# Kernel optimization log

Hardware: AMD Instinct MI355X
Metric: run time of the kernel (lower is better)

Reference implementation:

```python
import jax, jax.numpy as jnp
import numpy as np

H, DK, DV = 16, 64, 64

def setup_inputs() -> dict:
    key = jax.random.key(0)
    ks = jax.random.split(key, 5)
    S, E = 2048, 1024
    return {
        "x": jax.random.normal(ks[0], (S, E), jnp.float32),
        "Wq": jax.random.normal(ks[1], (H * DK, E), jnp.float32) * 0.02,
        "Wk": jax.random.normal(ks[2], (H * DK, E), jnp.float32) * 0.02,
        "Wv": jax.random.normal(ks[3], (H * DV, E), jnp.float32) * 0.02,
        "Wo": jax.random.normal(ks[4], (H * DV, H * DV), jnp.float32) * 0.02,
    }

def reference(x, Wq, Wk, Wv, Wo):
    S = x.shape[0]
    # Fused QKV projections (equivalent to per-head Linear with concatenated weights)
    Q = (x @ Wq.T).reshape(S, H, DK).transpose(1, 0, 2)  # [H,S,dk]
    K = (x @ Wk.T).reshape(S, H, DK).transpose(1, 0, 2)  # [H,S,dk]
    V = (x @ Wv.T).reshape(S, H, DV).transpose(1, 0, 2)  # [H,S,dv]
    scale = 1.0 / np.sqrt(DK).astype(np.float32)
    scores = jnp.einsum('hsd,htd->hst', Q, K) * scale    # [H,S,S]
    weights = jax.nn.softmax(scores, axis=-1)
    A = jnp.einsum('hst,htv->hsv', weights, V)           # [H,S,dv]
    A1 = A.transpose(1, 0, 2).reshape(S, H * DV)         # concat heads on last dim
    return A1 @ Wo.T
```

## Files before the change

kernel.cpp:

```cpp
#include <hip/hip_runtime.h>
#include <hip/hip_bf16.h>
#include <stdint.h>

typedef uint16_t u16;
typedef uint32_t u32;
typedef float    f32x4  __attribute__((ext_vector_type(4)));
typedef __bf16   bf16x8 __attribute__((ext_vector_type(8)));
typedef uint16_t u16x8  __attribute__((ext_vector_type(8)));
typedef uint16_t u16x4  __attribute__((ext_vector_type(4)));
typedef uint32_t u32x4  __attribute__((ext_vector_type(4)));

#define HH 16
#define SS 2048
#define EE 1024
#define DD 64

__device__ inline u16 f2bf(float f) {
  uint32_t u = __builtin_bit_cast(uint32_t, f);
  u += 0x7fff + ((u >> 16) & 1);
  return (u16)(u >> 16);
}
__device__ inline float bf2f(u16 b) {
  return __builtin_bit_cast(float, (uint32_t)b << 16);
}

__device__ inline u32 cvtpk(float lo, float hi) {
  u32 r;
  asm("v_cvt_pk_bf16_f32 %0, %1, %2" : "=v"(r) : "v"(lo), "v"(hi));
  return r;
}

__device__ inline void gload_lds16(const void* g, void* l) {
  __builtin_amdgcn_global_load_lds(
      (const __attribute__((address_space(1))) uint32_t*)g,
      (__attribute__((address_space(3))) uint32_t*)l, 16, 0, 0);
}

__global__ __launch_bounds__(256) void convert_kernel(
    const float* __restrict__ x,  const float* __restrict__ wq,
    const float* __restrict__ wk, const float* __restrict__ wv,
    const float* __restrict__ wo,
    u16* __restrict__ xb, u16* __restrict__ wqkvb, u16* __restrict__ wob) {
  const int64_t M1 = 1024 * 1024;
  int64_t e = ((int64_t)blockIdx.x * 256 + threadIdx.x) * 4;
  const float* src; u16* dst; int64_t off;
  if (e < 2 * M1)      { src = x;  dst = xb;           off = e; }
  else if (e < 3 * M1) { src = wq; dst = wqkvb;        off = e - 2 * M1; }
  else if (e < 4 * M1) { src = wk; dst = wqkvb + M1;   off = e - 3 * M1; }
  else if (e < 5 * M1) { src = wv; dst = wqkvb + 2*M1; off = e - 4 * M1; }
  else                 { src = wo; dst = wob;          off = e - 5 * M1; }
  float4 v = *(const float4*)(src + off);
  u16x4 o;
  o[0] = f2bf(v.x); o[1] = f2bf(v.y); o[2] = f2bf(v.z); o[3] = f2bf(v.w);
  *(u16x4*)(dst + off) = o;
}

template <int EPI, int K, int N>
__global__ __launch_bounds__(256, 4) void gemm_kernel(
    const u16* __restrict__ A, const u16* __restrict__ B,
    u16* __restrict__ q_ws, u16* __restrict__ k_ws, u16* __restrict__ vt_ws,
    float* __restrict__ Cout) {
  constexpr int BM = 64, BN = 128, BK = 64;
  __shared__ __align__(16) u16 As[BM * BK];
  __shared__ __align__(16) u16 Bs[BN * BK];
  const int t = threadIdx.x;
  const int lane = t & 63, w = t >> 6;
  const int wr = w >> 1, wc = w & 1;
  const int fr = lane & 15, fg = lane >> 4;

  const int nwg = gridDim.x * gridDim.y;
  const int bid = blockIdx.y * gridDim.x + blockIdx.x;
  const int swz = (bid & 7) * (nwg >> 3) + (bid >> 3);
  const int m0 = (swz / gridDim.x) * BM, n0 = (swz % gridDim.x) * BN;

  f32x4 acc[2][4] = {};

  for (int k0 = 0; k0 < K; k0 += BK) {
#pragma unroll
    for (int it = 0; it < 2; ++it) {
      const int c = t + it * 256, row = c >> 3, sch = (c & 7) ^ (row & 7);
      gload_lds16(A + (int64_t)(m0 + row) * K + k0 + sch * 8,
                  As + (c & ~63) * 8);
    }
#pragma unroll
    for (int it = 0; it < 4; ++it) {
      const int c = t + it * 256, row = c >> 3, sch = (c & 7) ^ (row & 7);
      gload_lds16(B + (int64_t)(n0 + row) * K + k0 + sch * 8,
                  Bs + (c & ~63) * 8);
    }
    __syncthreads();
    bf16x8 af[2][2], bfr[4][2];
#pragma unroll
    for (int mi = 0; mi < 2; ++mi)
#pragma unroll
      for (int kc = 0; kc < 2; ++kc) {
        const int row = wr * 32 + mi * 16 + fr;
        const int cc = (kc * 4 + fg) ^ (row & 7);
        af[mi][kc] = __builtin_bit_cast(bf16x8, *(const u16x8*)&As[row * 64 + cc * 8]);
      }
#pragma unroll
    for (int ni = 0; ni < 4; ++ni)
#pragma unroll
      for (int kc = 0; kc < 2; ++kc) {
        const int row = wc * 64 + ni * 16 + fr;
        const int cc = (kc * 4 + fg) ^ (row & 7);
        bfr[ni][kc] = __builtin_bit_cast(bf16x8, *(const u16x8*)&Bs[row * 64 + cc * 8]);
      }
#pragma unroll
    for (int kc = 0; kc < 2; ++kc)
#pragma unroll
      for (int mi = 0; mi < 2; ++mi)
#pragma unroll
        for (int ni = 0; ni < 4; ++ni)
          acc[mi][ni] = __builtin_amdgcn_mfma_f32_16x16x32_bf16(
              af[mi][kc], bfr[ni][kc], acc[mi][ni], 0, 0, 0);
    __syncthreads();
  }

#pragma unroll
  for (int mi = 0; mi < 2; ++mi)
#pragma unroll
    for (int ni = 0; ni < 4; ++ni)
#pragma unroll
      for (int r = 0; r < 4; ++r) {
        const int m = m0 + wr * 32 + mi * 16 + fg * 4 + r;
        const int n = n0 + wc * 64 + ni * 16 + fr;
        const float v = acc[mi][ni][r];
        if constexpr (EPI == 0) {
          const int which = n >> 10, nn = n & 1023, h = nn >> 6, d = nn & 63;
          const u16 bv = f2bf(v);
          if (which == 0)      q_ws[((int64_t)h * SS + m) * DD + d] = bv;
          else if (which == 1) k_ws[((int64_t)h * SS + m) * DD + d] = bv;
          else                 vt_ws[((int64_t)h * DD + d) * SS + m] = bv;
        } else {
          Cout[(int64_t)m * N + n] = v;
        }
      }
}

__global__ __launch_bounds__(256, 4) void attn_kernel(
    const u16* __restrict__ q_ws, const u16* __restrict__ k_ws,
    const u16* __restrict__ vt_ws, u16* __restrict__ opart,
    float2* __restrict__ ml) {
  constexpr int NT2 = SS / 64 / 2;
  __shared__ __align__(16) u16 lds[16384];
  const int t = threadIdx.x;
  const int lane = t & 63, w = t >> 6;
  const int ql = lane & 15, g = lane >> 4;
  const int h = blockIdx.y, qb = blockIdx.x, sp = blockIdx.z;
  const int kt0 = sp * NT2;
  const int qbase = qb * 64 + w * 16;

  const u16* Qh = q_ws + ((int64_t)h * SS + qbase) * DD;
  const u16* Kh = k_ws + ((int64_t)h * SS + kt0 * 64) * DD;
  const u16* Vh = vt_ws + (int64_t)h * DD * SS + kt0 * 64;

  const int r0 = t >> 3, ch = t & 7, r1 = (t + 256) >> 3;
  const int sch0 = ch ^ (r0 & 7), sch1 = ch ^ (r1 & 7);
  const int64_t ko0 = (int64_t)r0 * DD + sch0 * 8;
  const int64_t ko1 = (int64_t)r1 * DD + sch1 * 8;
  const int64_t vo0 = (int64_t)r0 * SS + sch0 * 8;
  const int64_t vo1 = (int64_t)r1 * SS + sch1 * 8;
  const int dst0 = (t & ~63) * 8, dst1 = (t & ~63) * 8 + 2048;

  bf16x8 qf[2];
#pragma unroll
  for (int dd = 0; dd < 2; ++dd)
    qf[dd] = __builtin_bit_cast(
        bf16x8, *(const u16x8*)(Qh + ql * DD + dd * 32 + g * 8));

  f32x4 o[4] = {};
  float m_run = -1e30f, l_run = 0.f;
  float sf = 1.f;
  const float C2 = 0.18033688f;

  auto qk = [&](f32x4 (&s)[4], const int kb_) {
    __builtin_amdgcn_s_setprio(1);
#pragma unroll
    for (int kb = 0; kb < 4; ++kb) {
      const int key = kb * 16 + ql;
      f32x4 z = {};
#pragma unroll
      for (int dd = 0; dd < 2; ++dd) {
        bf16x8 kf = __builtin_bit_cast(
            bf16x8,
            *(const u16x8*)&lds[kb_ * 4096 + key * 64 +
                                (((dd * 4 + g) ^ (ql & 7)) * 8)]);
        z = __builtin_amdgcn_mfma_f32_16x16x32_bf16(kf, qf[dd], z, 0, 0, 0);
      }
      s[kb] = z;
    }
    __builtin_amdgcn_s_setprio(0);
  };

  auto smpv = [&](f32x4 (&s)[4], const int vb_) {
    float m01 = fmaxf(fmaxf(s[0][0], s[0][1]), fmaxf(s[0][2], s[0][3]));
    float m23 = fmaxf(fmaxf(s[1][0], s[1][1]), fmaxf(s[1][2], s[1][3]));
    float m45 = fmaxf(fmaxf(s[2][0], s[2][1]), fmaxf(s[2][2], s[2][3]));
    float m67 = fmaxf(fmaxf(s[3][0], s[3][1]), fmaxf(s[3][2], s[3][3]));
    float mx = fmaxf(fmaxf(m01, m23), fmaxf(m45, m67));
    mx = fmaxf(mx, __shfl_xor(mx, 16));
    mx = fmaxf(mx, __shfl_xor(mx, 32));
    const float ts = mx * C2;
    const bool skip = __all(ts <= m_run + 8.0f);
    if (!skip) {
      const float mnew = fmaxf(m_run, ts);
      sf = exp2f(m_run - mnew);
      m_run = mnew;
    }
    float ls = 0.f;
#pragma unroll
    for (int kb = 0; kb < 4; ++kb)
#pragma unroll
      for (int r = 0; r < 4; ++r) {
        const float pv = exp2f(__fmaf_rn(s[kb][r], C2, -m_run));
        s[kb][r] = pv;
        ls += pv;
      }
    ls += __shfl_xor(ls, 16);
    ls += __shfl_xor(ls, 32);
    if (!skip) {
      l_run = __fmaf_rn(l_run, sf, ls);
#pragma unroll
      for (int r = 0; r < 4; ++r) {
        const float sfr = __shfl(sf, g * 4 + r);
#pragma unroll
        for (int nb = 0; nb < 4; ++nb) o[nb][r] *= sfr;
      }
    } else {
      l_run += ls;
    }
#pragma unroll
    for (int ks = 0; ks < 2; ++ks) {
      u32 x0 = cvtpk(s[2 * ks][0], s[2 * ks][1]);
      u32 x1 = cvtpk(s[2 * ks][2], s[2 * ks][3]);
      u32 y0 = cvtpk(s[2 * ks + 1][0], s[2 * ks + 1][1]);
      u32 y1 = cvtpk(s[2 * ks + 1][2], s[2 * ks + 1][3]);
      asm("v_permlane32_swap_b32 %0, %1" : "+v"(x0), "+v"(y0));
      asm("v_permlane16_swap_b32 %0, %1" : "+v"(x0), "+v"(y0));
      asm("v_permlane32_swap_b32 %0, %1" : "+v"(x1), "+v"(y1));
      asm("v_permlane16_swap_b32 %0, %1" : "+v"(x1), "+v"(y1));
      u32x4 aw; aw[0] = x0; aw[1] = x1; aw[2] = y0; aw[3] = y1;
      const bf16x8 pa = __builtin_bit_cast(bf16x8, aw);
      __builtin_amdgcn_s_setprio(1);
#pragma unroll
      for (int nb = 0; nb < 4; ++nb) {
        const int dv = nb * 16 + ql;
        bf16x8 vf = __builtin_bit_cast(
            bf16x8,
            *(const u16x8*)&lds[8192 + vb_ * 4096 + dv * 64 +
                                (((ks * 4 + g) ^ (ql & 7)) * 8)]);
        o[nb] = __builtin_amdgcn_mfma_f32_16x16x32_bf16(pa, vf, o[nb], 0, 0, 0);
      }
      __builtin_amdgcn_s_setprio(0);
    }
  };

  gload_lds16(Kh + ko0, lds + dst0);
  gload_lds16(Kh + ko1, lds + dst1);

  f32x4 sA[4], sB[4];
#pragma unroll
  for (int tt = 0; tt < NT2; ++tt) {
    __syncthreads();
    if (tt + 1 < NT2) {
      const u16* Kn = Kh + (int64_t)(tt + 1) * 64 * DD;
      const int kb = ((tt + 1) & 1) * 4096;
      gload_lds16(Kn + ko0, lds + kb + dst0);
      gload_lds16(Kn + ko1, lds + kb + dst1);
    }
    {
      const u16* Vn = Vh + tt * 64;
      const int vb = 8192 + (tt & 1) * 4096;
      gload_lds16(Vn + vo0, lds + vb + dst0);
      gload_lds16(Vn + vo1, lds + vb + dst1);
    }
    if (tt & 1) {
      qk(sB, tt & 1);
      smpv(sA, (tt - 1) & 1);
    } else {
      qk(sA, tt & 1);
      if (tt > 0) smpv(sB, (tt - 1) & 1);
    }
  }
  __syncthreads();
  smpv(sB, (NT2 - 1) & 1);

  const int64_t rowbase = ((int64_t)sp * HH + h) * SS;
#pragma unroll
  for (int r = 0; r < 4; ++r) {
    const int q = qbase + g * 4 + r;
#pragma unroll
    for (int nb = 0; nb < 4; ++nb)
      opart[(rowbase + q) * DD + nb * 16 + ql] = f2bf(o[nb][r]);
  }
  if (g == 0) ml[rowbase + qbase + ql] = make_float2(m_run, l_run);
}

__global__ __launch_bounds__(256) void combine_kernel(
    const u16* __restrict__ opart, const float2* __restrict__ ml,
    u16* __restrict__ a_ws) {
  const int rid = blockIdx.x * 4 + (threadIdx.x >> 6);
  const int lane = threadIdx.x & 63;
  const int h = rid >> 11, q = rid & 2047;
  const float2 ml1 = ml[rid];
  const float2 ml2 = ml[HH * SS + rid];
  const float m = fmaxf(ml1.x, ml2.x);
  const float a1 = exp2f(ml1.x - m), a2 = exp2f(ml2.x - m);
  const float inv = 1.0f / __fmaf_rn(a1, ml1.y, a2 * ml2.y);
  const float o1 = bf2f(opart[(int64_t)rid * DD + lane]);
  const float o2 = bf2f(opart[((int64_t)HH * SS + rid) * DD + lane]);
  a_ws[(int64_t)q * (HH * DD) + h * DD + lane] =
      f2bf((a1 * o1 + a2 * o2) * inv);
}

extern "C" void kernel_launch(void* const* d_in, const int* in_sizes, int n_in,
                              void* d_out, int out_size, void* d_ws, size_t ws_size,
                              hipStream_t stream) {
  const float* x  = (const float*)d_in[0];
  const float* wq = (const float*)d_in[1];
  const float* wk = (const float*)d_in[2];
  const float* wv = (const float*)d_in[3];
  const float* wo = (const float*)d_in[4];
  char* ws = (char*)d_ws;
  const int64_t Mi = 1 << 20;
  u16* xb    = (u16*)(ws + 0 * Mi);
  u16* wqkv  = (u16*)(ws + 4 * Mi);
  u16* q_ws  = (u16*)(ws + 12 * Mi);
  u16* k_ws  = (u16*)(ws + 16 * Mi);
  u16* vt    = (u16*)(ws + 20 * Mi);
  u16* wob   = (u16*)(ws + 24 * Mi);
  u16*    opart = (u16*)(ws + 0 * Mi);
  float2* mlv   = (float2*)(ws + 8 * Mi);
  u16* a_ws  = (u16*)(ws + 12 * Mi);
  float* out = (float*)d_out;

  convert_kernel<<<6144, 256, 0, stream>>>(x, wq, wk, wv, wo, xb, wqkv, wob);

  gemm_kernel<0, 1024, 3072><<<dim3(3072 / 128, 2048 / 64), 256, 0, stream>>>(
      xb, wqkv, q_ws, k_ws, vt, nullptr);

  attn_kernel<<<dim3(SS / 64, HH, 2), 256, 0, stream>>>(q_ws, k_ws, vt, opart, mlv);

  combine_kernel<<<HH * SS / 4, 256, 0, stream>>>(opart, mlv, a_ws);

  gemm_kernel<1, 1024, 1024><<<dim3(1024 / 128, 2048 / 64), 256, 0, stream>>>(
      a_ws, wob, nullptr, nullptr, nullptr, out);
}
```

Measured before the change: 92.74 us.

## Split attention KV range four ways and stage partials in output buffer

Attention now splits the key/value sequence into four chunks instead of two, which doubles the grid and halves the loop length per block. Occupancy hint rises from 4 to 5 blocks per SM. The extra partial outputs go to the output buffer as scratch, since workspace space is limited, and the combine kernel merges four partials. The intent is more parallelism and shorter serial loops per block, at the cost of more partial-output traffic and combine work.

```diff
diff --git a/kernel.cpp b/kernel.cpp
--- a/kernel.cpp
+++ b/kernel.cpp
@@ -138,17 +138,17 @@
       }
 }
 
-__global__ __launch_bounds__(256, 4) void attn_kernel(
+__global__ __launch_bounds__(256, 5) void attn_kernel(
     const u16* __restrict__ q_ws, const u16* __restrict__ k_ws,
-    const u16* __restrict__ vt_ws, u16* __restrict__ opart,
-    float2* __restrict__ ml) {
-  constexpr int NT2 = SS / 64 / 2;
+    const u16* __restrict__ vt_ws, u16* __restrict__ ob_lo,
+    u16* __restrict__ ob_hi, float2* __restrict__ ml) {
+  constexpr int NTS = SS / 64 / 4;
   __shared__ __align__(16) u16 lds[16384];
   const int t = threadIdx.x;
   const int lane = t & 63, w = t >> 6;
   const int ql = lane & 15, g = lane >> 4;
   const int h = blockIdx.y, qb = blockIdx.x, sp = blockIdx.z;
-  const int kt0 = sp * NT2;
+  const int kt0 = sp * NTS;
   const int qbase = qb * 64 + w * 16;
 
   const u16* Qh = q_ws + ((int64_t)h * SS + qbase) * DD;
@@ -161,7 +161,7 @@
   const int64_t ko1 = (int64_t)r1 * DD + sch1 * 8;
   const int64_t vo0 = (int64_t)r0 * SS + sch0 * 8;
   const int64_t vo1 = (int64_t)r1 * SS + sch1 * 8;
-  const int dst0 = (t & ~63) * 8, dst1 = (t & ~63) * 8 + 2048;
+  const int dst0 = (t & ~63) * 8, dst1 = dst0 + 2048;
 
   bf16x8 qf[2];
 #pragma unroll
@@ -194,11 +194,10 @@
   };
 
   auto smpv = [&](f32x4 (&s)[4], const int vb_) {
-    float m01 = fmaxf(fmaxf(s[0][0], s[0][1]), fmaxf(s[0][2], s[0][3]));
-    float m23 = fmaxf(fmaxf(s[1][0], s[1][1]), fmaxf(s[1][2], s[1][3]));
-    float m45 = fmaxf(fmaxf(s[2][0], s[2][1]), fmaxf(s[2][2], s[2][3]));
-    float m67 = fmaxf(fmaxf(s[3][0], s[3][1]), fmaxf(s[3][2], s[3][3]));
-    float mx = fmaxf(fmaxf(m01, m23), fmaxf(m45, m67));
+    float mx = fmaxf(fmaxf(s[0][0], s[0][1]), fmaxf(s[0][2], s[0][3]));
+    mx = fmaxf(mx, fmaxf(fmaxf(s[1][0], s[1][1]), fmaxf(s[1][2], s[1][3])));
+    mx = fmaxf(mx, fmaxf(fmaxf(s[2][0], s[2][1]), fmaxf(s[2][2], s[2][3])));
+    mx = fmaxf(mx, fmaxf(fmaxf(s[3][0], s[3][1]), fmaxf(s[3][2], s[3][3])));
     mx = fmaxf(mx, __shfl_xor(mx, 16));
     mx = fmaxf(mx, __shfl_xor(mx, 32));
     const float ts = mx * C2;
@@ -261,9 +260,9 @@
 
   f32x4 sA[4], sB[4];
 #pragma unroll
-  for (int tt = 0; tt < NT2; ++tt) {
+  for (int tt = 0; tt < NTS; ++tt) {
     __syncthreads();
-    if (tt + 1 < NT2) {
+    if (tt + 1 < NTS) {
       const u16* Kn = Kh + (int64_t)(tt + 1) * 64 * DD;
       const int kb = ((tt + 1) & 1) * 4096;
       gload_lds16(Kn + ko0, lds + kb + dst0);
@@ -284,34 +283,41 @@
     }
   }
   __syncthreads();
-  smpv(sB, (NT2 - 1) & 1);
-
-  const int64_t rowbase = ((int64_t)sp * HH + h) * SS;
+  smpv(sB, (NTS - 1) & 1);
+
+  u16* ob = (sp & 2) ? ob_hi : ob_lo;
+  const int64_t rowbase = ((int64_t)(sp & 1) * HH + h) * SS;
 #pragma unroll
   for (int r = 0; r < 4; ++r) {
     const int q = qbase + g * 4 + r;
 #pragma unroll
     for (int nb = 0; nb < 4; ++nb)
-      opart[(rowbase + q) * DD + nb * 16 + ql] = f2bf(o[nb][r]);
+      ob[(rowbase + q) * DD + nb * 16 + ql] = f2bf(o[nb][r]);
   }
-  if (g == 0) ml[rowbase + qbase + ql] = make_float2(m_run, l_run);
+  if (g == 0)
+    ml[((int64_t)sp * HH + h) * SS + qbase + ql] = make_float2(m_run, l_run);
 }
 
 __global__ __launch_bounds__(256) void combine_kernel(
-    const u16* __restrict__ opart, const float2* __restrict__ ml,
-    u16* __restrict__ a_ws) {
+    const u16* __restrict__ olo, const u16* __restrict__ ohi,
+    const float2* __restrict__ ml, u16* __restrict__ a_ws) {
   const int rid = blockIdx.x * 4 + (threadIdx.x >> 6);
   const int lane = threadIdx.x & 63;
   const int h = rid >> 11, q = rid & 2047;
-  const float2 ml1 = ml[rid];
-  const float2 ml2 = ml[HH * SS + rid];
-  const float m = fmaxf(ml1.x, ml2.x);
-  const float a1 = exp2f(ml1.x - m), a2 = exp2f(ml2.x - m);
-  const float inv = 1.0f / __fmaf_rn(a1, ml1.y, a2 * ml2.y);
-  const float o1 = bf2f(opart[(int64_t)rid * DD + lane]);
-  const float o2 = bf2f(opart[((int64_t)HH * SS + rid) * DD + lane]);
+  const float2 l0 = ml[rid];
+  const float2 l1 = ml[HH * SS + rid];
+  const float2 l2 = ml[2 * HH * SS + rid];
+  const float2 l3 = ml[3 * HH * SS + rid];
+  const float m = fmaxf(fmaxf(l0.x, l1.x), fmaxf(l2.x, l3.x));
+  const float a0 = exp2f(l0.x - m), a1 = exp2f(l1.x - m);
+  const float a2 = exp2f(l2.x - m), a3 = exp2f(l3.x - m);
+  const float inv = 1.0f / (a0 * l0.y + a1 * l1.y + a2 * l2.y + a3 * l3.y);
+  const float o0 = bf2f(olo[(int64_t)rid * DD + lane]);
+  const float o1 = bf2f(olo[((int64_t)HH * SS + rid) * DD + lane]);
+  const float o2 = bf2f(ohi[(int64_t)rid * DD + lane]);
+  const float o3 = bf2f(ohi[((int64_t)HH * SS + rid) * DD + lane]);
   a_ws[(int64_t)q * (HH * DD) + h * DD + lane] =
-      f2bf((a1 * o1 + a2 * o2) * inv);
+      f2bf((a0 * o0 + a1 * o1 + a2 * o2 + a3 * o3) * inv);
 }
 
 extern "C" void kernel_launch(void* const* d_in, const int* in_sizes, int n_in,
@@ -326,12 +332,13 @@
   const int64_t Mi = 1 << 20;
   u16* xb    = (u16*)(ws + 0 * Mi);
   u16* wqkv  = (u16*)(ws + 4 * Mi);
+  u16* wob   = (u16*)(ws + 10 * Mi);
   u16* q_ws  = (u16*)(ws + 12 * Mi);
   u16* k_ws  = (u16*)(ws + 16 * Mi);
   u16* vt    = (u16*)(ws + 20 * Mi);
-  u16* wob   = (u16*)(ws + 24 * Mi);
-  u16*    opart = (u16*)(ws + 0 * Mi);
-  float2* mlv   = (float2*)(ws + 8 * Mi);
+  u16*    olo = (u16*)(ws + 0 * Mi);
+  u16*    ohi = (u16*)d_out;
+  float2* mlv = (float2*)(ws + 8 * Mi);
   u16* a_ws  = (u16*)(ws + 12 * Mi);
   float* out = (float*)d_out;
 
@@ -340,9 +347,10 @@
   gemm_kernel<0, 1024, 3072><<<dim3(3072 / 128, 2048 / 64), 256, 0, stream>>>(
       xb, wqkv, q_ws, k_ws, vt, nullptr);
 
-  attn_kernel<<<dim3(SS / 64, HH, 2), 256, 0, stream>>>(q_ws, k_ws, vt, opart, mlv);
-
-  combine_kernel<<<HH * SS / 4, 256, 0, stream>>>(opart, mlv, a_ws);
+  attn_kernel<<<dim3(SS / 64, HH, 4), 256, 0, stream>>>(
+      q_ws, k_ws, vt, olo, ohi, mlv);
+
+  combine_kernel<<<HH * SS / 4, 256, 0, stream>>>(olo, ohi, mlv, a_ws);
 
   gemm_kernel<1, 1024, 1024><<<dim3(1024 / 128, 2048 / 64), 256, 0, stream>>>(
       a_ws, wob, nullptr, nullptr, nullptr, out);
```

Measured after the change: 96.94 us. 4.5% more time.
